# Kernel optimization log

Measured on AMD Instinct MI355X. Metric: run time of the kernel, lower is better.

Reference implementation:

```python
import jax, jax.numpy as jnp
import numpy as np

KERNEL = 8
STRIDE = 4
K_LIST = [KERNEL // 2, KERNEL, KERNEL + KERNEL // 2]  # [4, 8, 12]


def _unfold(x, k, s):
    # x: (N, C, H, W) -> (N, L, C, k, k), windows row-major (h outer, w inner)
    N, C, H, W = x.shape
    oh = (H - k) // s + 1
    ow = (W - k) // s + 1
    rows = (jnp.arange(oh) * s)[:, None] + jnp.arange(k)  # (oh, k)
    cols = (jnp.arange(ow) * s)[:, None] + jnp.arange(k)  # (ow, k)
    # advanced indexing broadcast -> (N, C, oh, ow, k, k)
    p = x[:, :, rows[:, None, :, None], cols[None, :, None, :]]
    return p.transpose(0, 2, 3, 1, 4, 5).reshape(N, oh * ow, C, k, k)


def _adaptive_avg_mat(n_in, n_out):
    # PyTorch adaptive_avg_pool1d bin edges: [floor(i*n_in/n_out), ceil((i+1)*n_in/n_out))
    M = np.zeros((n_out, n_in), dtype=np.float32)
    for i in range(n_out):
        s = (i * n_in) // n_out
        e = -((-(i + 1) * n_in) // n_out)
        M[i, s:e] = 1.0 / (e - s)
    return jnp.asarray(M)


def setup_inputs() -> dict:
    key = jax.random.key(0)
    k1, k2, k3 = jax.random.split(key, 3)
    x = jax.random.normal(k1, (8, 64, 256, 256), dtype=jnp.float32)
    w_reduce = jax.random.normal(k2, (16, 64), dtype=jnp.float32) / np.sqrt(64.0)
    b_reduce = jax.random.normal(k3, (16,), dtype=jnp.float32) * 0.01
    return {"x": x, "w_reduce": w_reduce, "b_reduce": b_reduce}


def reference(x, w_reduce, b_reduce):
    N, C, H, W = x.shape
    # crop to even H, W
    x = x[:, :, : H - (H % 2), : W - (W % 2)]
    # replicate pad by 1 on each side
    x = jnp.pad(x, ((0, 0), (0, 0), (1, 1), (1, 1)), mode="edge")
    # 1x1 conv reduce: C -> C // 4
    x = jnp.einsum("nchw,oc->nohw", x, w_reduce) + b_reduce[None, :, None, None]

    outs = []
    for k in K_LIST:
        p = _unfold(x, k, STRIDE)  # (N, L, Cr, k, k)
        Nn, L, Cr = p.shape[:3]
        if k < KERNEL:
            # bilinear upsample (align_corners=False, half-pixel centers)
            p = jax.image.resize(
                p.reshape(Nn * L, Cr, k, k),
                (Nn * L, Cr, KERNEL, KERNEL),
                method="bilinear",
            ).reshape(Nn, L, Cr, KERNEL, KERNEL)
        elif k > KERNEL:
            M = _adaptive_avg_mat(k, KERNEL)  # (KERNEL, k)
            p = jnp.einsum("nlcij,pi,qj->nlcpq", p, M, M)
        outs.append(p)
    # concat along the window dimension
    return jnp.concatenate(outs, axis=1)  # (N, 11909, Cr, 8, 8)
```

## Files before the change

### kernel.cpp

```cpp
#include <hip/hip_runtime.h>

#define C_IN 64
#define C_OUT 16
#define H 256
#define W 256
#define HW 65536
#define N_B 8
#define L4 4096
#define L8 3969
#define L12 3844
#define LTOT 11909
#define LDSP 260

typedef float float4u __attribute__((ext_vector_type(4), aligned(4)));
typedef float f4v __attribute__((ext_vector_type(4)));

__device__ __forceinline__ void nt_store4(const float4& v, float* p) {
  f4v t; t.x = v.x; t.y = v.y; t.z = v.z; t.w = v.w;
  __builtin_nontemporal_store(t, reinterpret_cast<f4v*>(p));
}

__device__ __forceinline__ float4 load4c(const float* __restrict__ row, int ws0) {
  if (ws0 >= 0) {
    float4u t = *reinterpret_cast<const float4u*>(row + ws0);
    return make_float4(t.x, t.y, t.z, t.w);
  }
  return make_float4(row[0], row[0], row[1], row[2]);
}

__global__ __launch_bounds__(256) void reduce_kernel(
    const float* __restrict__ x, const float* __restrict__ w,
    const float* __restrict__ b, float* __restrict__ y) {
  __shared__ float wt[C_IN][C_OUT];
  for (int i = threadIdx.x; i < C_IN * C_OUT; i += 256)
    wt[i & 63][i >> 6] = w[i];
  __syncthreads();

  const unsigned gid = blockIdx.x * 256 + threadIdx.x;
  const int n = gid >> 14;
  const int pix = (gid & 16383) << 2;
  const float* xp = x + (size_t)n * C_IN * HW + pix;

  float4 acc[C_OUT];
#pragma unroll
  for (int o = 0; o < C_OUT; ++o) {
    const float bv = b[o];
    acc[o] = make_float4(bv, bv, bv, bv);
  }

#define FMA4(A, WS) \
  A.x = fmaf(xv.x, WS, A.x); A.y = fmaf(xv.y, WS, A.y); \
  A.z = fmaf(xv.z, WS, A.z); A.w = fmaf(xv.w, WS, A.w);

#pragma unroll
  for (int c = 0; c < C_IN; ++c) {
    const float4 xv = *reinterpret_cast<const float4*>(xp + (size_t)c * HW);
    const float4 w0 = *reinterpret_cast<const float4*>(&wt[c][0]);
    const float4 w1 = *reinterpret_cast<const float4*>(&wt[c][4]);
    const float4 w2 = *reinterpret_cast<const float4*>(&wt[c][8]);
    const float4 w3 = *reinterpret_cast<const float4*>(&wt[c][12]);
    FMA4(acc[0], w0.x)  FMA4(acc[1], w0.y)  FMA4(acc[2], w0.z)  FMA4(acc[3], w0.w)
    FMA4(acc[4], w1.x)  FMA4(acc[5], w1.y)  FMA4(acc[6], w1.z)  FMA4(acc[7], w1.w)
    FMA4(acc[8], w2.x)  FMA4(acc[9], w2.y)  FMA4(acc[10], w2.z) FMA4(acc[11], w2.w)
    FMA4(acc[12], w3.x) FMA4(acc[13], w3.y) FMA4(acc[14], w3.z) FMA4(acc[15], w3.w)
  }
#undef FMA4

  float* yp = y + (size_t)n * C_OUT * HW + pix;
#pragma unroll
  for (int o = 0; o < C_OUT; ++o)
    *reinterpret_cast<float4*>(yp + (size_t)o * HW) = acc[o];
}


__global__ __launch_bounds__(256) void patch4_kernel(
    const float* __restrict__ y, float* __restrict__ out) {
  const int CP = 4 * LDSP + 8;
  __shared__ float lds[4 * (4 * LDSP + 8)];
  const int bid = blockIdx.x;
  const int oh = bid & 63;
  const int cq = (bid >> 6) & 3;
  const int n = bid >> 8;
  const int tid = threadIdx.x;

#pragma unroll
  for (int i = 0; i < 4; ++i) {
    const int sid = i * 256 + tid;
    const int c = sid >> 8;
    const int t = (sid >> 6) & 3;
    const int k = sid & 63;
    const int r = min(max(oh * 4 + t - 1, 0), H - 1);
    const float4 v = load4c(y + (size_t)(n * C_OUT + cq * 4 + c) * HW + (size_t)r * W, 4 * k - 1);
    *reinterpret_cast<float4*>(&lds[c * CP + t * LDSP + 4 * k]) = v;
  }
  __syncthreads();

  const int lane = tid & 63;
  const int c = lane >> 4;
  const int p = (lane >> 1) & 7;
  const int qh = lane & 1;
  const int lrow = tid >> 6;

  const int ip0 = max(0, (p - 1) >> 1), ip1 = min(3, (p + 1) >> 1);
  const float wp0 = (p == 0 || p == 7) ? 1.0f : ((p & 1) ? 0.75f : 0.25f);
  const float wp1 = 1.0f - wp0;
  const float* lr0 = &lds[c * CP + ip0 * LDSP];
  const float* lr1 = &lds[c * CP + ip1 * LDSP];
  float* ob = out + ((size_t)(n * LTOT + oh * 64) * C_OUT + cq * 4 + c) * 64 + p * 8 + qh * 4;

#pragma unroll
  for (int i = 0; i < 16; ++i) {
    const int ow = i * 4 + lrow;
    const float4 A = *reinterpret_cast<const float4*>(lr0 + ow * 4);
    const float4 B = *reinterpret_cast<const float4*>(lr1 + ow * 4);
    float4 ta, tb;
    if (qh == 0) {
      ta = make_float4(A.x, 0.75f * A.x + 0.25f * A.y, 0.25f * A.x + 0.75f * A.y, 0.75f * A.y + 0.25f * A.z);
      tb = make_float4(B.x, 0.75f * B.x + 0.25f * B.y, 0.25f * B.x + 0.75f * B.y, 0.75f * B.y + 0.25f * B.z);
    } else {
      ta = make_float4(0.25f * A.y + 0.75f * A.z, 0.75f * A.z + 0.25f * A.w, 0.25f * A.z + 0.75f * A.w, A.w);
      tb = make_float4(0.25f * B.y + 0.75f * B.z, 0.75f * B.z + 0.25f * B.w, 0.25f * B.z + 0.75f * B.w, B.w);
    }
    const float4 v = make_float4(wp0 * ta.x + wp1 * tb.x, wp0 * ta.y + wp1 * tb.y,
                                 wp0 * ta.z + wp1 * tb.z, wp0 * ta.w + wp1 * tb.w);
    nt_store4(v, ob + (size_t)ow * (C_OUT * 64));
  }
}

__global__ __launch_bounds__(256) void patch8_kernel(
    const float* __restrict__ y, float* __restrict__ out) {
  const int CP = 8 * LDSP + 8;
  __shared__ float lds[4 * (8 * LDSP + 8)];
  const int bid = blockIdx.x;
  const int oh = bid % 63;
  const int cqn = bid / 63;
  const int cq = cqn & 3;
  const int n = cqn >> 2;
  const int tid = threadIdx.x;

#pragma unroll
  for (int i = 0; i < 8; ++i) {
    const int sid = i * 256 + tid;
    const int c = sid >> 9;
    const int t = (sid >> 6) & 7;
    const int k = sid & 63;
    const int r = min(max(oh * 4 + t - 1, 0), H - 1);
    const float4 v = load4c(y + (size_t)(n * C_OUT + cq * 4 + c) * HW + (size_t)r * W, 4 * k - 1);
    *reinterpret_cast<float4*>(&lds[c * CP + t * LDSP + 4 * k]) = v;
  }
  __syncthreads();

  const int lane = tid & 63;
  const int c = lane >> 4;
  const int p = (lane >> 1) & 7;
  const int qh = lane & 1;
  const int lrow = tid >> 6;

  const float* lr = &lds[c * CP + p * LDSP + qh * 4];
  float* ob = out + ((size_t)(n * LTOT + L4 + oh * 63) * C_OUT + cq * 4 + c) * 64 + p * 8 + qh * 4;

#pragma unroll
  for (int i = 0; i < 16; ++i) {
    const int ow = i * 4 + lrow;
    if (ow < 63) {
      const float4 v = *reinterpret_cast<const float4*>(lr + ow * 4);
      nt_store4(v, ob + (size_t)ow * (C_OUT * 64));
    }
  }
}

__global__ __launch_bounds__(256) void patch12_kernel(
    const float* __restrict__ y, float* __restrict__ out) {
  const int CP = 12 * LDSP + 8;
  __shared__ float lds[4 * (12 * LDSP + 8)];
  const int bid = blockIdx.x;
  const int oh = bid % 62;
  const int cqn = bid / 62;
  const int cq = cqn & 3;
  const int n = cqn >> 2;
  const int tid = threadIdx.x;

#pragma unroll
  for (int i = 0; i < 12; ++i) {
    const int sid = i * 256 + tid;
    const int c = sid / 768;
    const int rem = sid - c * 768;
    const int t = rem >> 6;
    const int k = rem & 63;
    const int r = min(max(oh * 4 + t - 1, 0), H - 1);
    const float4 v = load4c(y + (size_t)(n * C_OUT + cq * 4 + c) * HW + (size_t)r * W, 4 * k - 1);
    *reinterpret_cast<float4*>(&lds[c * CP + t * LDSP + 4 * k]) = v;
  }
  __syncthreads();

  const int lane = tid & 63;
  const int c = lane >> 4;
  const int p = (lane >> 1) & 7;
  const int qh = lane & 1;
  const int lrow = tid >> 6;

  const int a = (3 * p) >> 1;
  const float* r0 = &lds[c * CP + a * LDSP];
  const float* r1 = r0 + LDSP;
  float* ob = out + ((size_t)(n * LTOT + L4 + L8 + oh * 62) * C_OUT + cq * 4 + c) * 64 + p * 8 + qh * 4;

#pragma unroll
  for (int i = 0; i < 16; ++i) {
    const int ow = i * 4 + lrow;
    if (ow < 62) {
      const float4 F40 = *reinterpret_cast<const float4*>(r0 + ow * 4 + qh * 8);
      const float2 F20 = *reinterpret_cast<const float2*>(r0 + ow * 4 + 4 + qh * 2);
      const float4 F41 = *reinterpret_cast<const float4*>(r1 + ow * 4 + qh * 8);
      const float2 F21 = *reinterpret_cast<const float2*>(r1 + ow * 4 + 4 + qh * 2);
      const float e0 = qh ? F20.x : F40.x, f0 = qh ? F21.x : F41.x;
      const float e1 = qh ? F20.y : F40.y, f1 = qh ? F21.y : F41.y;
      const float e2 = qh ? F40.x : F40.z, f2 = qh ? F41.x : F41.z;
      const float e3 = qh ? F40.y : F40.w, f3 = qh ? F41.y : F41.w;
      const float e4 = qh ? F40.z : F20.x, f4 = qh ? F41.z : F21.x;
      const float e5 = qh ? F40.w : F20.y, f5 = qh ? F41.w : F21.y;
      const float4 v = make_float4(0.25f * (e0 + e1 + f0 + f1),
                                   0.25f * (e1 + e2 + f1 + f2),
                                   0.25f * (e3 + e4 + f3 + f4),
                                   0.25f * (e4 + e5 + f4 + f5));
      nt_store4(v, ob + (size_t)ow * (C_OUT * 64));
    }
  }
}

extern "C" void kernel_launch(void* const* d_in, const int* in_sizes, int n_in,
                              void* d_out, int out_size, void* d_ws, size_t ws_size,
                              hipStream_t stream) {
  const float* x = (const float*)d_in[0];
  const float* w = (const float*)d_in[1];
  const float* b = (const float*)d_in[2];
  float* out = (float*)d_out;
  float* y = (float*)d_ws;

  reduce_kernel<<<512, 256, 0, stream>>>(x, w, b, y);
  patch4_kernel<<<N_B * 4 * 64, 256, 0, stream>>>(y, out);
  patch8_kernel<<<N_B * 4 * 63, 256, 0, stream>>>(y, out);
  patch12_kernel<<<N_B * 4 * 62, 256, 0, stream>>>(y, out);
}
```

Measured before the change: 127.6 us.

## Fuse the three patch-extraction kernels into one kernel sharing a 12-row LDS tile

Replaces the separate k=4, k=8 and k=12 patch kernels with one kernel per (batch, channel quad, output row). It loads a single 12-row tile of the reduced feature map into LDS and emits all three window scales from it. This removes two kernel launches and the repeated global reads of overlapping rows of y. In exchange every block loads 12 rows and uses the larger LDS footprint, which may lower occupancy for the k=4 part, and each block now does more serial work.

```diff
diff --git a/kernel.cpp b/kernel.cpp
--- a/kernel.cpp
+++ b/kernel.cpp
@@ -72,112 +72,14 @@
     *reinterpret_cast<float4*>(yp + (size_t)o * HW) = acc[o];
 }
 
-
-__global__ __launch_bounds__(256) void patch4_kernel(
+__global__ __launch_bounds__(256) void patch_fused_kernel(
     const float* __restrict__ y, float* __restrict__ out) {
-  const int CP = 4 * LDSP + 8;
-  __shared__ float lds[4 * (4 * LDSP + 8)];
+  const int CP = 12 * LDSP + 8;
+  __shared__ float lds[4 * (12 * LDSP + 8)];
   const int bid = blockIdx.x;
   const int oh = bid & 63;
   const int cq = (bid >> 6) & 3;
   const int n = bid >> 8;
-  const int tid = threadIdx.x;
-
-#pragma unroll
-  for (int i = 0; i < 4; ++i) {
-    const int sid = i * 256 + tid;
-    const int c = sid >> 8;
-    const int t = (sid >> 6) & 3;
-    const int k = sid & 63;
-    const int r = min(max(oh * 4 + t - 1, 0), H - 1);
-    const float4 v = load4c(y + (size_t)(n * C_OUT + cq * 4 + c) * HW + (size_t)r * W, 4 * k - 1);
-    *reinterpret_cast<float4*>(&lds[c * CP + t * LDSP + 4 * k]) = v;
-  }
-  __syncthreads();
-
-  const int lane = tid & 63;
-  const int c = lane >> 4;
-  const int p = (lane >> 1) & 7;
-  const int qh = lane & 1;
-  const int lrow = tid >> 6;
-
-  const int ip0 = max(0, (p - 1) >> 1), ip1 = min(3, (p + 1) >> 1);
-  const float wp0 = (p == 0 || p == 7) ? 1.0f : ((p & 1) ? 0.75f : 0.25f);
-  const float wp1 = 1.0f - wp0;
-  const float* lr0 = &lds[c * CP + ip0 * LDSP];
-  const float* lr1 = &lds[c * CP + ip1 * LDSP];
-  float* ob = out + ((size_t)(n * LTOT + oh * 64) * C_OUT + cq * 4 + c) * 64 + p * 8 + qh * 4;
-
-#pragma unroll
-  for (int i = 0; i < 16; ++i) {
-    const int ow = i * 4 + lrow;
-    const float4 A = *reinterpret_cast<const float4*>(lr0 + ow * 4);
-    const float4 B = *reinterpret_cast<const float4*>(lr1 + ow * 4);
-    float4 ta, tb;
-    if (qh == 0) {
-      ta = make_float4(A.x, 0.75f * A.x + 0.25f * A.y, 0.25f * A.x + 0.75f * A.y, 0.75f * A.y + 0.25f * A.z);
-      tb = make_float4(B.x, 0.75f * B.x + 0.25f * B.y, 0.25f * B.x + 0.75f * B.y, 0.75f * B.y + 0.25f * B.z);
-    } else {
-      ta = make_float4(0.25f * A.y + 0.75f * A.z, 0.75f * A.z + 0.25f * A.w, 0.25f * A.z + 0.75f * A.w, A.w);
-      tb = make_float4(0.25f * B.y + 0.75f * B.z, 0.75f * B.z + 0.25f * B.w, 0.25f * B.z + 0.75f * B.w, B.w);
-    }
-    const float4 v = make_float4(wp0 * ta.x + wp1 * tb.x, wp0 * ta.y + wp1 * tb.y,
-                                 wp0 * ta.z + wp1 * tb.z, wp0 * ta.w + wp1 * tb.w);
-    nt_store4(v, ob + (size_t)ow * (C_OUT * 64));
-  }
-}
-
-__global__ __launch_bounds__(256) void patch8_kernel(
-    const float* __restrict__ y, float* __restrict__ out) {
-  const int CP = 8 * LDSP + 8;
-  __shared__ float lds[4 * (8 * LDSP + 8)];
-  const int bid = blockIdx.x;
-  const int oh = bid % 63;
-  const int cqn = bid / 63;
-  const int cq = cqn & 3;
-  const int n = cqn >> 2;
-  const int tid = threadIdx.x;
-
-#pragma unroll
-  for (int i = 0; i < 8; ++i) {
-    const int sid = i * 256 + tid;
-    const int c = sid >> 9;
-    const int t = (sid >> 6) & 7;
-    const int k = sid & 63;
-    const int r = min(max(oh * 4 + t - 1, 0), H - 1);
-    const float4 v = load4c(y + (size_t)(n * C_OUT + cq * 4 + c) * HW + (size_t)r * W, 4 * k - 1);
-    *reinterpret_cast<float4*>(&lds[c * CP + t * LDSP + 4 * k]) = v;
-  }
-  __syncthreads();
-
-  const int lane = tid & 63;
-  const int c = lane >> 4;
-  const int p = (lane >> 1) & 7;
-  const int qh = lane & 1;
-  const int lrow = tid >> 6;
-
-  const float* lr = &lds[c * CP + p * LDSP + qh * 4];
-  float* ob = out + ((size_t)(n * LTOT + L4 + oh * 63) * C_OUT + cq * 4 + c) * 64 + p * 8 + qh * 4;
-
-#pragma unroll
-  for (int i = 0; i < 16; ++i) {
-    const int ow = i * 4 + lrow;
-    if (ow < 63) {
-      const float4 v = *reinterpret_cast<const float4*>(lr + ow * 4);
-      nt_store4(v, ob + (size_t)ow * (C_OUT * 64));
-    }
-  }
-}
-
-__global__ __launch_bounds__(256) void patch12_kernel(
-    const float* __restrict__ y, float* __restrict__ out) {
-  const int CP = 12 * LDSP + 8;
-  __shared__ float lds[4 * (12 * LDSP + 8)];
-  const int bid = blockIdx.x;
-  const int oh = bid % 62;
-  const int cqn = bid / 62;
-  const int cq = cqn & 3;
-  const int n = cqn >> 2;
   const int tid = threadIdx.x;
 
 #pragma unroll
@@ -198,31 +100,74 @@
   const int p = (lane >> 1) & 7;
   const int qh = lane & 1;
   const int lrow = tid >> 6;
+  const float* lc = &lds[c * CP];
+  const size_t obase = ((size_t)n * LTOT) * (C_OUT * 64) + (size_t)(cq * 4 + c) * 64 + p * 8 + qh * 4;
 
-  const int a = (3 * p) >> 1;
-  const float* r0 = &lds[c * CP + a * LDSP];
-  const float* r1 = r0 + LDSP;
-  float* ob = out + ((size_t)(n * LTOT + L4 + L8 + oh * 62) * C_OUT + cq * 4 + c) * 64 + p * 8 + qh * 4;
+  {
+    const int ip0 = max(0, (p - 1) >> 1), ip1 = min(3, (p + 1) >> 1);
+    const float wp0 = (p == 0 || p == 7) ? 1.0f : ((p & 1) ? 0.75f : 0.25f);
+    const float wp1 = 1.0f - wp0;
+    const float* lr0 = lc + ip0 * LDSP;
+    const float* lr1 = lc + ip1 * LDSP;
+    float* ob = out + obase + (size_t)(oh * 64) * (C_OUT * 64);
 
 #pragma unroll
-  for (int i = 0; i < 16; ++i) {
-    const int ow = i * 4 + lrow;
-    if (ow < 62) {
-      const float4 F40 = *reinterpret_cast<const float4*>(r0 + ow * 4 + qh * 8);
-      const float2 F20 = *reinterpret_cast<const float2*>(r0 + ow * 4 + 4 + qh * 2);
-      const float4 F41 = *reinterpret_cast<const float4*>(r1 + ow * 4 + qh * 8);
-      const float2 F21 = *reinterpret_cast<const float2*>(r1 + ow * 4 + 4 + qh * 2);
-      const float e0 = qh ? F20.x : F40.x, f0 = qh ? F21.x : F41.x;
-      const float e1 = qh ? F20.y : F40.y, f1 = qh ? F21.y : F41.y;
-      const float e2 = qh ? F40.x : F40.z, f2 = qh ? F41.x : F41.z;
-      const float e3 = qh ? F40.y : F40.w, f3 = qh ? F41.y : F41.w;
-      const float e4 = qh ? F40.z : F20.x, f4 = qh ? F41.z : F21.x;
-      const float e5 = qh ? F40.w : F20.y, f5 = qh ? F41.w : F21.y;
-      const float4 v = make_float4(0.25f * (e0 + e1 + f0 + f1),
-                                   0.25f * (e1 + e2 + f1 + f2),
-                                   0.25f * (e3 + e4 + f3 + f4),
-                                   0.25f * (e4 + e5 + f4 + f5));
+    for (int i = 0; i < 16; ++i) {
+      const int ow = i * 4 + lrow;
+      const float4 A = *reinterpret_cast<const float4*>(lr0 + ow * 4);
+      const float4 B = *reinterpret_cast<const float4*>(lr1 + ow * 4);
+      float4 ta, tb;
+      if (qh == 0) {
+        ta = make_float4(A.x, 0.75f * A.x + 0.25f * A.y, 0.25f * A.x + 0.75f * A.y, 0.75f * A.y + 0.25f * A.z);
+        tb = make_float4(B.x, 0.75f * B.x + 0.25f * B.y, 0.25f * B.x + 0.75f * B.y, 0.75f * B.y + 0.25f * B.z);
+      } else {
+        ta = make_float4(0.25f * A.y + 0.75f * A.z, 0.75f * A.z + 0.25f * A.w, 0.25f * A.z + 0.75f * A.w, A.w);
+        tb = make_float4(0.25f * B.y + 0.75f * B.z, 0.75f * B.z + 0.25f * B.w, 0.25f * B.z + 0.75f * B.w, B.w);
+      }
+      const float4 v = make_float4(wp0 * ta.x + wp1 * tb.x, wp0 * ta.y + wp1 * tb.y,
+                                   wp0 * ta.z + wp1 * tb.z, wp0 * ta.w + wp1 * tb.w);
       nt_store4(v, ob + (size_t)ow * (C_OUT * 64));
+    }
+  }
+
+  if (oh < 63) {
+    const float* lr = lc + p * LDSP + qh * 4;
+    float* ob = out + obase + (size_t)(L4 + oh * 63) * (C_OUT * 64);
+#pragma unroll
+    for (int i = 0; i < 16; ++i) {
+      const int ow = i * 4 + lrow;
+      if (ow < 63) {
+        const float4 v = *reinterpret_cast<const float4*>(lr + ow * 4);
+        nt_store4(v, ob + (size_t)ow * (C_OUT * 64));
+      }
+    }
+  }
+
+  if (oh < 62) {
+    const int a = (3 * p) >> 1;
+    const float* r0 = lc + a * LDSP;
+    const float* r1 = r0 + LDSP;
+    float* ob = out + obase + (size_t)(L4 + L8 + oh * 62) * (C_OUT * 64);
+#pragma unroll
+    for (int i = 0; i < 16; ++i) {
+      const int ow = i * 4 + lrow;
+      if (ow < 62) {
+        const float4 F40 = *reinterpret_cast<const float4*>(r0 + ow * 4 + qh * 8);
+        const float2 F20 = *reinterpret_cast<const float2*>(r0 + ow * 4 + 4 + qh * 2);
+        const float4 F41 = *reinterpret_cast<const float4*>(r1 + ow * 4 + qh * 8);
+        const float2 F21 = *reinterpret_cast<const float2*>(r1 + ow * 4 + 4 + qh * 2);
+        const float e0 = qh ? F20.x : F40.x, f0 = qh ? F21.x : F41.x;
+        const float e1 = qh ? F20.y : F40.y, f1 = qh ? F21.y : F41.y;
+        const float e2 = qh ? F40.x : F40.z, f2 = qh ? F41.x : F41.z;
+        const float e3 = qh ? F40.y : F40.w, f3 = qh ? F41.y : F41.w;
+        const float e4 = qh ? F40.z : F20.x, f4 = qh ? F41.z : F21.x;
+        const float e5 = qh ? F40.w : F20.y, f5 = qh ? F41.w : F21.y;
+        const float4 v = make_float4(0.25f * (e0 + e1 + f0 + f1),
+                                     0.25f * (e1 + e2 + f1 + f2),
+                                     0.25f * (e3 + e4 + f3 + f4),
+                                     0.25f * (e4 + e5 + f4 + f5));
+        nt_store4(v, ob + (size_t)ow * (C_OUT * 64));
+      }
     }
   }
 }
@@ -237,7 +182,5 @@
   float* y = (float*)d_ws;
 
   reduce_kernel<<<512, 256, 0, stream>>>(x, w, b, y);
-  patch4_kernel<<<N_B * 4 * 64, 256, 0, stream>>>(y, out);
-  patch8_kernel<<<N_B * 4 * 63, 256, 0, stream>>>(y, out);
-  patch12_kernel<<<N_B * 4 * 62, 256, 0, stream>>>(y, out);
+  patch_fused_kernel<<<N_B * 4 * 64, 256, 0, stream>>>(y, out);
 }
```

Result: faster. 109.4 us (-14.3%).
